# Kernel optimization log

Hardware: AMD Instinct MI355X
Metric: run time of the kernel (lower is better)

The kernel has to match this reference:

```python
import jax, jax.numpy as jnp
import numpy as np

B, S, H, I, E, K = 2, 512, 1024, 4096, 8, 2
LN_EPS = 1e-5


def setup_inputs() -> dict:
    key = jax.random.key(0)
    ks = jax.random.split(key, 5)
    sc = 0.02  # init scale for weights
    return {
        "hidden_states": jax.random.normal(ks[0], (B, S, H), jnp.float32),
        "ln_w": jnp.ones((H,), jnp.float32),
        "ln_b": jnp.zeros((H,), jnp.float32),
        "Wr": jax.random.normal(ks[1], (E, H), jnp.float32) * sc,  # router [out=E, in=H]
        "br": jnp.zeros((E,), jnp.float32),
        "W1": jax.random.normal(ks[2], (E, I, H), jnp.float32) * sc,  # dense1 per expert [out=I, in=H]
        "b1": jnp.zeros((E, I), jnp.float32),
        "W2": jax.random.normal(ks[3], (E, H, I), jnp.float32) * sc,  # dense2 per expert [out=H, in=I]
        "b2": jnp.zeros((E, H), jnp.float32),
    }


def reference(hidden_states, ln_w, ln_b, Wr, br, W1, b1, W2, b2):
    # Eval mode: no jitter noise, no dropout.
    residual = hidden_states
    mu = jnp.mean(hidden_states, axis=-1, keepdims=True)
    var = jnp.mean(jnp.square(hidden_states - mu), axis=-1, keepdims=True)
    x = (hidden_states - mu) * jax.lax.rsqrt(var + LN_EPS) * ln_w + ln_b  # [B,S,H]

    logits = jnp.einsum("bsh,eh->bse", x, Wr) + br  # [B,S,E]
    topw, topi = jax.lax.top_k(logits, K)  # [B,S,K]
    topw = jax.nn.softmax(topw, axis=-1)
    # Combine weights per expert (top-k indices are distinct, so scatter == first-match)
    combine = jnp.sum(jax.nn.one_hot(topi, E, dtype=x.dtype) * topw[..., None], axis=-2)  # [B,S,E]

    # Dense per-expert FFN (reference form of gather-FFN-scatter); combine zeros out unselected experts
    a = jax.nn.gelu(jnp.einsum("bsh,eih->bsei", x, W1) + b1, approximate=False)  # [B,S,E,I]
    y = jnp.einsum("bsei,ehi->bseh", a, W2) + b2  # [B,S,E,H]
    out = residual + jnp.einsum("bse,bseh->bsh", combine, y)

    probs = jax.nn.softmax(logits, axis=-1)
    usage = jnp.mean(probs, axis=(0, 1))  # [E]
    balance_loss = E * jnp.sum(usage * usage) - 1.0
    return out, balance_loss
```

## Files before the change

kernel.cpp:

```cpp
#include <hip/hip_runtime.h>
#include <hip/hip_bf16.h>
#include <math.h>
#include <stdint.h>

#define T_TOK 1024
#define H_DIM 1024
#define I_DIM 4096
#define E_NUM 8
#define NSLOT (2 * T_TOK)
#define WELEM 33554432
#define MAXT 24

typedef __attribute__((ext_vector_type(8))) short bf16x8;
typedef __attribute__((ext_vector_type(4))) float f32x4;

#define MFMA_BF16(a, b, c) __builtin_amdgcn_mfma_f32_16x16x32_bf16(a, b, c, 0, 0, 0)

__device__ __forceinline__ short f2bf(float f) {
  union { float f; unsigned u; } x; x.f = f;
  unsigned r = (x.u + 0x7fffu + ((x.u >> 16) & 1u)) >> 16;
  return (short)r;
}
__device__ __forceinline__ int pack2bf(float a, float b) {
  return ((int)(unsigned short)f2bf(a)) | (((int)f2bf(b)) << 16);
}

typedef __attribute__((address_space(3))) unsigned int as3_u32;
typedef const __attribute__((address_space(1))) unsigned int as1_u32c;
__device__ __forceinline__ void glds16(const void* g, void* l) {
  __builtin_amdgcn_global_load_lds((as1_u32c*)g, (as3_u32*)l, 16, 0, 0);
}

union BBCast { int4 i4; bf16x8 v; };

__device__ __forceinline__ void cvtpack_dev(const float* __restrict__ src,
                                            short* __restrict__ dst,
                                            int bid, int nb, int rsh, int csh) {
  const size_t total8 = ((size_t)E_NUM << (rsh + csh)) >> 3;
  const int kmask = (1 << (csh - 3)) - 1;
  const int nmask = (1 << rsh) - 1;
  for (size_t id = (size_t)bid * 256 + threadIdx.x; id < total8;
       id += (size_t)nb * 256) {
    int k8 = (int)(id & kmask);
    int n = (int)((id >> (csh - 3)) & nmask);
    int e = (int)(id >> (csh - 3 + rsh));
    int k = k8 << 3;
    size_t eoff = (size_t)e << (rsh + csh);
    const float* s = src + eoff + ((size_t)n << csh) + k;
    float4 a = *(const float4*)s;
    float4 b = *(const float4*)(s + 4);
    int4 p;
    p.x = pack2bf(a.x, a.y); p.y = pack2bf(a.z, a.w);
    p.z = pack2bf(b.x, b.y); p.w = pack2bf(b.z, b.w);
    size_t tile = ((size_t)(n >> 7) << (csh - 5)) + (k >> 5);
    *(int4*)(dst + eoff + tile * 4096 + ((n & 127) << 5) + (k & 31)) = p;
  }
}

__global__ __launch_bounds__(256) void k_pre(
    const float* __restrict__ x, const float* __restrict__ ln_w,
    const float* __restrict__ ln_b, const float* __restrict__ Wr,
    const float* __restrict__ br,
    short* __restrict__ xln, int* __restrict__ sel_e, float* __restrict__ sel_w,
    float* __restrict__ probs, float* __restrict__ out,
    const float* __restrict__ W1src, short* __restrict__ w1dst, int ncvt) {
  __shared__ float sx[H_DIM];
  __shared__ float redS[8];
  __shared__ float slog[E_NUM];

  if (blockIdx.x >= T_TOK) {
    cvtpack_dev(W1src, w1dst, blockIdx.x - T_TOK, ncvt, 12, 10);
    return;
  }
  const int t = blockIdx.x;
  const int tid = threadIdx.x;
  const int lane = tid & 63, wid = tid >> 6;

  float4 v = ((const float4*)(x + (size_t)t * H_DIM))[tid];
  ((float4*)(out + (size_t)t * H_DIM))[tid] = v;
  float s = v.x + v.y + v.z + v.w;
  float ss = v.x * v.x + v.y * v.y + v.z * v.z + v.w * v.w;
  for (int o = 32; o > 0; o >>= 1) { s += __shfl_down(s, o); ss += __shfl_down(ss, o); }
  if (lane == 0) { redS[wid] = s; redS[4 + wid] = ss; }
  __syncthreads();
  float st = redS[0] + redS[1] + redS[2] + redS[3];
  float sst = redS[4] + redS[5] + redS[6] + redS[7];
  float mu = st * (1.0f / H_DIM);
  float var = sst * (1.0f / H_DIM) - mu * mu;
  float rs = rsqrtf(var + 1e-5f);

  float4 lw = ((const float4*)ln_w)[tid];
  float4 lb = ((const float4*)ln_b)[tid];
  float4 xn;
  xn.x = (v.x - mu) * rs * lw.x + lb.x;
  xn.y = (v.y - mu) * rs * lw.y + lb.y;
  xn.z = (v.z - mu) * rs * lw.z + lb.z;
  xn.w = (v.w - mu) * rs * lw.w + lb.w;
  sx[4 * tid + 0] = xn.x; sx[4 * tid + 1] = xn.y;
  sx[4 * tid + 2] = xn.z; sx[4 * tid + 3] = xn.w;
  short4 s4;
  s4.x = f2bf(xn.x); s4.y = f2bf(xn.y); s4.z = f2bf(xn.z); s4.w = f2bf(xn.w);
  ((short4*)(xln + (size_t)t * H_DIM))[tid] = s4;
  __syncthreads();

  for (int e = 2 * wid; e < 2 * wid + 2; ++e) {
    float p = 0.f;
    for (int h = lane; h < H_DIM; h += 64) p += sx[h] * Wr[e * H_DIM + h];
    for (int o = 32; o > 0; o >>= 1) p += __shfl_down(p, o);
    if (lane == 0) slog[e] = p + br[e];
  }
  __syncthreads();

  if (tid == 0) {
    float lg[E_NUM];
    for (int e = 0; e < E_NUM; ++e) lg[e] = slog[e];
    int i0 = 0;
    for (int e = 1; e < E_NUM; ++e) if (lg[e] > lg[i0]) i0 = e;
    int i1 = (i0 == 0) ? 1 : 0;
    for (int e = 0; e < E_NUM; ++e) if (e != i0 && lg[e] > lg[i1]) i1 = e;
    float w1e = __expf(lg[i1] - lg[i0]);
    float den = 1.f + w1e;
    sel_e[2 * t] = i0; sel_w[2 * t] = 1.f / den;
    sel_e[2 * t + 1] = i1; sel_w[2 * t + 1] = w1e / den;
    float se = 0.f, pe[E_NUM];
    for (int e = 0; e < E_NUM; ++e) { pe[e] = __expf(lg[e] - lg[i0]); se += pe[e]; }
    float inv = 1.f / se;
    for (int e = 0; e < E_NUM; ++e) probs[t * E_NUM + e] = pe[e] * inv;
  }
}

__global__ __launch_bounds__(512) void k_route(
    const int* __restrict__ sel_e, const float* __restrict__ sel_w,
    const float* __restrict__ probs,
    int* __restrict__ counts, int* __restrict__ basep,
    int* __restrict__ tile_e, int* __restrict__ tile_m0, int* __restrict__ ntiles,
    int* __restrict__ tlist, int* __restrict__ sel_idx,
    float* __restrict__ wslot, float* __restrict__ loss_out) {
  const int wid = threadIdx.x >> 6;
  const int lane = threadIdx.x & 63;
  __shared__ int scnt[E_NUM];
  __shared__ float susage[E_NUM];

  int cnt = 0;
  for (int s0 = 0; s0 < NSLOT; s0 += 64) {
    int s = s0 + lane;
    bool m = (sel_e[s] == wid);
    unsigned long long mk = __ballot(m);
    int pre = __popcll(mk & ((1ULL << lane) - 1ULL));
    if (m) {
      int idx = cnt + pre;
      sel_idx[s] = idx;
      tlist[wid * T_TOK + idx] = s >> 1;
      wslot[wid * T_TOK + idx] = sel_w[s];
    }
    cnt += __popcll(mk);
  }
  if (lane == 0) scnt[wid] = cnt;

  float u = 0.f;
  for (int t = lane; t < T_TOK; t += 64) u += probs[t * E_NUM + wid];
  for (int o = 32; o > 0; o >>= 1) u += __shfl_down(u, o);
  if (lane == 0) susage[wid] = u * (1.0f / T_TOK);
  __syncthreads();

  if (threadIdx.x == 0) {
    int b = 0, nt = 0;
    for (int e = 0; e < E_NUM; ++e) {
      basep[e] = b; counts[e] = scnt[e];
      int te = (scnt[e] + 127) >> 7;
      for (int i = 0; i < te && nt < MAXT; ++i) {
        tile_e[nt] = e; tile_m0[nt] = i * 128; ++nt;
      }
      b += te * 128;
    }
    ntiles[0] = nt;
    float sq = 0.f;
    for (int e = 0; e < E_NUM; ++e) sq += susage[e] * susage[e];
    *loss_out = (float)E_NUM * sq - 1.0f;
  }
}

__global__ __launch_bounds__(256) void k_cvtpack(const float* __restrict__ src,
                                                 short* __restrict__ dst,
                                                 int rsh, int csh) {
  cvtpack_dev(src, dst, blockIdx.x, gridDim.x, rsh, csh);
}

__global__ __launch_bounds__(256) void k_ffn1(
    const short* __restrict__ xln, const short* __restrict__ W1b,
    const float* __restrict__ b1, const int* __restrict__ counts,
    const int* __restrict__ basep,
    const int* __restrict__ tile_e, const int* __restrict__ tile_m0,
    const int* __restrict__ ntiles, const int* __restrict__ tlist,
    short* __restrict__ a_buf,
    const float* __restrict__ W2src, short* __restrict__ w2dst) {
  const int bid = blockIdx.x;
  if (bid >= MAXT * 32) {
    cvtpack_dev(W2src, w2dst, bid - MAXT * 32, gridDim.x - MAXT * 32, 10, 12);
    return;
  }
  const int tileid = bid >> 5;
  if (tileid >= ntiles[0]) return;
  const int e = tile_e[tileid];
  const int m0 = tile_m0[tileid];
  const int cnt = counts[e];
  const int n0 = (bid & 31) * 128;

  __shared__ __align__(16) short As[3][128 * 32];
  __shared__ __align__(16) short Bs[3][128 * 32];

  const int tid = threadIdx.x;
  const int lane = tid & 63, wid = tid >> 6;
  const int wr = wid >> 1, wc = wid & 1;
  const int fr = lane & 15, fq = lane >> 4;

  int r0 = m0 + (tid >> 2); if (r0 >= cnt) r0 = cnt - 1;
  int r1 = m0 + 64 + (tid >> 2); if (r1 >= cnt) r1 = cnt - 1;
  const short* ag0 = xln + (size_t)tlist[e * T_TOK + r0] * H_DIM + (tid & 3) * 8;
  const short* ag1 = xln + (size_t)tlist[e * T_TOK + r1] * H_DIM + (tid & 3) * 8;
  const short* bgp = W1b + ((size_t)e << 22) + ((size_t)(n0 >> 7) * 131072) + tid * 8;

  f32x4 acc[4][4];
#pragma unroll
  for (int i = 0; i < 4; ++i)
#pragma unroll
    for (int j = 0; j < 4; ++j) acc[i][j] = (f32x4)0.f;

#define STAGE(kt, buf)                                          \
  {                                                             \
    glds16(ag0 + (kt) * 32, &As[buf][tid * 8]);                 \
    glds16(ag1 + (kt) * 32, &As[buf][(256 + tid) * 8]);         \
    glds16(bgp + (size_t)(kt) * 4096, &Bs[buf][tid * 8]);       \
    glds16(bgp + (size_t)(kt) * 4096 + 2048,                    \
           &Bs[buf][(256 + tid) * 8]);                          \
  }

  STAGE(0, 0);
  STAGE(1, 1);

  const int KT = H_DIM / 32;
  for (int kt = 0; kt < KT; ++kt) {
    if (kt == KT - 1) {
      asm volatile("s_waitcnt vmcnt(0)" ::: "memory");
    } else {
      asm volatile("s_waitcnt vmcnt(4)" ::: "memory");
    }
    __builtin_amdgcn_s_barrier();
    if (kt + 2 < KT) STAGE(kt + 2, (kt + 2) % 3);
    const int cb = kt % 3;
    bf16x8 af[4], bb[4];
#pragma unroll
    for (int mi = 0; mi < 4; ++mi)
      af[mi] = *(const bf16x8*)&As[cb][(wr * 64 + mi * 16 + fr) * 32 + fq * 8];
#pragma unroll
    for (int ni = 0; ni < 4; ++ni)
      bb[ni] = *(const bf16x8*)&Bs[cb][(wc * 64 + ni * 16 + fr) * 32 + fq * 8];
#pragma unroll
    for (int mi = 0; mi < 4; ++mi)
#pragma unroll
      for (int ni = 0; ni < 4; ++ni)
        acc[mi][ni] = MFMA_BF16(af[mi], bb[ni], acc[mi][ni]);
  }
#undef STAGE

  const size_t T1 = (size_t)(basep[e] + m0) >> 7;
  short* abase = a_buf + T1 * 524288;
  float b1v[4];
#pragma unroll
  for (int ni = 0; ni < 4; ++ni)
    b1v[ni] = b1[e * I_DIM + n0 + wc * 64 + ni * 16 + fr];
#pragma unroll
  for (int mi = 0; mi < 4; ++mi)
#pragma unroll
    for (int j = 0; j < 4; ++j) {
      int r = wr * 64 + mi * 16 + fq * 4 + j;
      if (m0 + r < cnt) {
#pragma unroll
        for (int ni = 0; ni < 4; ++ni) {
          int colg = n0 + wc * 64 + ni * 16 + fr;
          float vv = acc[mi][ni][j] + b1v[ni];
          float g = 0.5f * vv * (1.0f + erff(vv * 0.70710678118654752f));
          abase[(size_t)(colg >> 5) * 4096 + r * 32 + (colg & 31)] = f2bf(g);
        }
      }
    }
}

__global__ __launch_bounds__(256) void k_ffn2(
    const short* __restrict__ a_buf, const short* __restrict__ W2b,
    const float* __restrict__ b2, const int* __restrict__ counts,
    const int* __restrict__ basep,
    const int* __restrict__ tile_e, const int* __restrict__ tile_m0,
    const int* __restrict__ ntiles, const int* __restrict__ tlist,
    const float* __restrict__ wslot, float* __restrict__ out) {
  const int bid = blockIdx.x;
  const int tileid = bid >> 5;
  if (tileid >= ntiles[0]) return;
  const int rem = bid & 31;
  const int kc = rem >> 3;
  const int n0 = (rem & 7) * 128;
  const int e = tile_e[tileid];
  const int m0 = tile_m0[tileid];
  const int cnt = counts[e];

  __shared__ __align__(16) short As[3][128 * 32];
  __shared__ __align__(16) short Bs[3][128 * 32];

  const int tid = threadIdx.x;
  const int lane = tid & 63, wid = tid >> 6;
  const int wr = wid >> 1, wc = wid & 1;
  const int fr = lane & 15, fq = lane >> 4;

  const size_t T1 = (size_t)(basep[e] + m0) >> 7;
  const short* agp = a_buf + T1 * 524288 + (size_t)kc * 131072 + tid * 8;
  const short* bgp = W2b + ((size_t)e << 22) + ((size_t)(n0 >> 7) * 524288) +
                     (size_t)kc * 131072 + tid * 8;

  f32x4 acc[4][4];
#pragma unroll
  for (int i = 0; i < 4; ++i)
#pragma unroll
    for (int j = 0; j < 4; ++j) acc[i][j] = (f32x4)0.f;

#define STAGE(kt, buf)                                          \
  {                                                             \
    glds16(agp + (size_t)(kt) * 4096, &As[buf][tid * 8]);       \
    glds16(agp + (size_t)(kt) * 4096 + 2048,                    \
           &As[buf][(256 + tid) * 8]);                          \
    glds16(bgp + (size_t)(kt) * 4096, &Bs[buf][tid * 8]);       \
    glds16(bgp + (size_t)(kt) * 4096 + 2048,                    \
           &Bs[buf][(256 + tid) * 8]);                          \
  }

  STAGE(0, 0);
  STAGE(1, 1);

  const int KT = 32;
  for (int kt = 0; kt < KT; ++kt) {
    if (kt == KT - 1) {
      asm volatile("s_waitcnt vmcnt(0)" ::: "memory");
    } else {
      asm volatile("s_waitcnt vmcnt(4)" ::: "memory");
    }
    __builtin_amdgcn_s_barrier();
    if (kt + 2 < KT) STAGE(kt + 2, (kt + 2) % 3);
    const int cb = kt % 3;
    bf16x8 af[4], bb[4];
#pragma unroll
    for (int mi = 0; mi < 4; ++mi)
      af[mi] = *(const bf16x8*)&As[cb][(wr * 64 + mi * 16 + fr) * 32 + fq * 8];
#pragma unroll
    for (int ni = 0; ni < 4; ++ni)
      bb[ni] = *(const bf16x8*)&Bs[cb][(wc * 64 + ni * 16 + fr) * 32 + fq * 8];
#pragma unroll
    for (int mi = 0; mi < 4; ++mi)
#pragma unroll
      for (int ni = 0; ni < 4; ++ni)
        acc[mi][ni] = MFMA_BF16(af[mi], bb[ni], acc[mi][ni]);
  }
#undef STAGE

  float b2v[4];
#pragma unroll
  for (int ni = 0; ni < 4; ++ni)
    b2v[ni] = 0.25f * b2[e * H_DIM + n0 + wc * 64 + ni * 16 + fr];
#pragma unroll
  for (int mi = 0; mi < 4; ++mi)
#pragma unroll
    for (int j = 0; j < 4; ++j) {
      int r = wr * 64 + mi * 16 + fq * 4 + j;
      if (m0 + r < cnt) {
        int tok = tlist[e * T_TOK + m0 + r];
        float w = wslot[e * T_TOK + m0 + r];
        float* orow = out + (size_t)tok * H_DIM;
#pragma unroll
        for (int ni = 0; ni < 4; ++ni) {
          int colg = n0 + wc * 64 + ni * 16 + fr;
          atomicAdd(&orow[colg], w * (acc[mi][ni][j] + b2v[ni]));
        }
      }
    }
}

__global__ __launch_bounds__(256) void k_ffn1_f32(
    const short* __restrict__ xln, const float* __restrict__ W1,
    const float* __restrict__ b1, const int* __restrict__ counts,
    const int* __restrict__ basep, const int* __restrict__ tlist,
    short* __restrict__ a_buf) {
  const int e = blockIdx.z;
  const int cnt = counts[e];
  const int m0 = blockIdx.y * 128;
  if (m0 >= cnt) return;
  const int n0 = blockIdx.x * 128;
  __shared__ __align__(16) short As[2][128 * 32];
  __shared__ __align__(16) float Bsf[2][128 * 32];
  const int tid = threadIdx.x;
  const int lane = tid & 63, wid = tid >> 6;
  const int wr = wid >> 1, wc = wid & 1;
  const int fr = lane & 15, fq = lane >> 4;
  int r0 = m0 + (tid >> 2); if (r0 >= cnt) r0 = cnt - 1;
  int r1 = m0 + 64 + (tid >> 2); if (r1 >= cnt) r1 = cnt - 1;
  const short* ag0 = xln + (size_t)tlist[e * T_TOK + r0] * H_DIM + (tid & 3) * 8;
  const short* ag1 = xln + (size_t)tlist[e * T_TOK + r1] * H_DIM + (tid & 3) * 8;
  const int bro = tid >> 3;
  const int bslot = (tid & 7) ^ (bro & 7);
  const float* bg = W1 + ((size_t)e * I_DIM + n0 + bro) * H_DIM + bslot * 4;
  f32x4 acc[4][4];
#pragma unroll
  for (int i = 0; i < 4; ++i)
#pragma unroll
    for (int j = 0; j < 4; ++j) acc[i][j] = (f32x4)0.f;
#define STAGE(kk, buf)                                                      \
  {                                                                         \
    glds16(ag0 + (kk), &As[buf][tid * 8]);                                  \
    glds16(ag1 + (kk), &As[buf][(256 + tid) * 8]);                          \
    _Pragma("unroll") for (int i = 0; i < 4; ++i)                           \
        glds16(bg + (size_t)(i * 32) * H_DIM + (kk),                        \
               &Bsf[buf][(i * 256 + tid) * 4]);                             \
  }
  STAGE(0, 0);
  __syncthreads();
  int cur = 0;
  for (int kt = 0; kt < H_DIM / 32; ++kt) {
    if (kt + 1 < H_DIM / 32) STAGE((kt + 1) * 32, cur ^ 1);
    bf16x8 af[4], bb[4];
#pragma unroll
    for (int mi = 0; mi < 4; ++mi)
      af[mi] = *(const bf16x8*)&As[cur][(wr * 64 + mi * 16 + fr) * 32 + fq * 8];
#pragma unroll
    for (int ni = 0; ni < 4; ++ni) {
      const int row = wc * 64 + ni * 16 + fr;
      const int base = row * 128 + fq * 32;
      const int sw = (row & 7) << 4;
      f32x4 lo = *(const f32x4*)((const char*)&Bsf[cur][0] + (base ^ sw));
      f32x4 hi = *(const f32x4*)((const char*)&Bsf[cur][0] + ((base + 16) ^ sw));
      BBCast c;
      c.i4.x = pack2bf(lo[0], lo[1]); c.i4.y = pack2bf(lo[2], lo[3]);
      c.i4.z = pack2bf(hi[0], hi[1]); c.i4.w = pack2bf(hi[2], hi[3]);
      bb[ni] = c.v;
    }
#pragma unroll
    for (int mi = 0; mi < 4; ++mi)
#pragma unroll
      for (int ni = 0; ni < 4; ++ni)
        acc[mi][ni] = MFMA_BF16(af[mi], bb[ni], acc[mi][ni]);
    __syncthreads();
    cur ^= 1;
  }
#undef STAGE
  const int slot0 = basep[e] + m0;
  float b1v[4];
#pragma unroll
  for (int ni = 0; ni < 4; ++ni)
    b1v[ni] = b1[e * I_DIM + n0 + wc * 64 + ni * 16 + fr];
#pragma unroll
  for (int mi = 0; mi < 4; ++mi)
#pragma unroll
    for (int j = 0; j < 4; ++j) {
      int r = wr * 64 + mi * 16 + fq * 4 + j;
      if (m0 + r < cnt) {
        size_t rowoff = (size_t)(slot0 + r) * I_DIM;
#pragma unroll
        for (int ni = 0; ni < 4; ++ni) {
          int colg = n0 + wc * 64 + ni * 16 + fr;
          float vv = acc[mi][ni][j] + b1v[ni];
          float g = 0.5f * vv * (1.0f + erff(vv * 0.70710678118654752f));
          a_buf[rowoff + colg] = f2bf(g);
        }
      }
    }
}

__global__ __launch_bounds__(256) void k_ffn2_f32(
    const short* __restrict__ a_buf, const float* __restrict__ W2,
    const float* __restrict__ b2, const int* __restrict__ counts,
    const int* __restrict__ basep, const int* __restrict__ tlist,
    const float* __restrict__ wslot, float* __restrict__ out, int lg) {
  const int z = blockIdx.z;
  const int e = z >> lg;
  const int kc = z & ((1 << lg) - 1);
  const int CH = I_DIM >> lg;
  const int cnt = counts[e];
  const int m0 = blockIdx.y * 128;
  if (m0 >= cnt) return;
  const int n0 = blockIdx.x * 128;
  __shared__ __align__(16) short As[2][128 * 32];
  __shared__ __align__(16) float Bsf[2][128 * 32];
  const int tid = threadIdx.x;
  const int lane = tid & 63, wid = tid >> 6;
  const int wr = wid >> 1, wc = wid & 1;
  const int fr = lane & 15, fq = lane >> 4;
  int r0 = m0 + (tid >> 2); if (r0 >= cnt) r0 = cnt - 1;
  int r1 = m0 + 64 + (tid >> 2); if (r1 >= cnt) r1 = cnt - 1;
  const int sb = basep[e];
  const short* ag0 = a_buf + (size_t)(sb + r0) * I_DIM + kc * CH + (tid & 3) * 8;
  const short* ag1 = a_buf + (size_t)(sb + r1) * I_DIM + kc * CH + (tid & 3) * 8;
  const int bro = tid >> 3;
  const int bslot = (tid & 7) ^ (bro & 7);
  const float* bg = W2 + ((size_t)e * H_DIM + n0 + bro) * I_DIM + kc * CH + bslot * 4;
  f32x4 acc[4][4];
#pragma unroll
  for (int i = 0; i < 4; ++i)
#pragma unroll
    for (int j = 0; j < 4; ++j) acc[i][j] = (f32x4)0.f;
#define STAGE(kk, buf)                                                      \
  {                                                                         \
    glds16(ag0 + (kk), &As[buf][tid * 8]);                                  \
    glds16(ag1 + (kk), &As[buf][(256 + tid) * 8]);                          \
    _Pragma("unroll") for (int i = 0; i < 4; ++i)                           \
        glds16(bg + (size_t)(i * 32) * I_DIM + (kk),                        \
               &Bsf[buf][(i * 256 + tid) * 4]);                             \
  }
  STAGE(0, 0);
  __syncthreads();
  const int KT = CH / 32;
  int cur = 0;
  for (int kt = 0; kt < KT; ++kt) {
    if (kt + 1 < KT) STAGE((kt + 1) * 32, cur ^ 1);
    bf16x8 af[4], bb[4];
#pragma unroll
    for (int mi = 0; mi < 4; ++mi)
      af[mi] = *(const bf16x8*)&As[cur][(wr * 64 + mi * 16 + fr) * 32 + fq * 8];
#pragma unroll
    for (int ni = 0; ni < 4; ++ni) {
      const int row = wc * 64 + ni * 16 + fr;
      const int base = row * 128 + fq * 32;
      const int sw = (row & 7) << 4;
      f32x4 lo = *(const f32x4*)((const char*)&Bsf[cur][0] + (base ^ sw));
      f32x4 hi = *(const f32x4*)((const char*)&Bsf[cur][0] + ((base + 16) ^ sw));
      BBCast c;
      c.i4.x = pack2bf(lo[0], lo[1]); c.i4.y = pack2bf(lo[2], lo[3]);
      c.i4.z = pack2bf(hi[0], hi[1]); c.i4.w = pack2bf(hi[2], hi[3]);
      bb[ni] = c.v;
    }
#pragma unroll
    for (int mi = 0; mi < 4; ++mi)
#pragma unroll
      for (int ni = 0; ni < 4; ++ni)
        acc[mi][ni] = MFMA_BF16(af[mi], bb[ni], acc[mi][ni]);
    __syncthreads();
    cur ^= 1;
  }
#undef STAGE
  const float inv = 1.0f / (float)(1 << lg);
  float b2v[4];
#pragma unroll
  for (int ni = 0; ni < 4; ++ni)
    b2v[ni] = inv * b2[e * H_DIM + n0 + wc * 64 + ni * 16 + fr];
#pragma unroll
  for (int mi = 0; mi < 4; ++mi)
#pragma unroll
    for (int j = 0; j < 4; ++j) {
      int r = wr * 64 + mi * 16 + fq * 4 + j;
      if (m0 + r < cnt) {
        int tok = tlist[e * T_TOK + m0 + r];
        float w = wslot[e * T_TOK + m0 + r];
        float* orow = out + (size_t)tok * H_DIM;
#pragma unroll
        for (int ni = 0; ni < 4; ++ni) {
          int colg = n0 + wc * 64 + ni * 16 + fr;
          atomicAdd(&orow[colg], w * (acc[mi][ni][j] + b2v[ni]));
        }
      }
    }
}

extern "C" void kernel_launch(void* const* d_in, const int* in_sizes, int n_in,
                              void* d_out, int out_size, void* d_ws, size_t ws_size,
                              hipStream_t stream) {
  const float* hidden = (const float*)d_in[0];
  const float* ln_w = (const float*)d_in[1];
  const float* ln_b = (const float*)d_in[2];
  const float* Wr = (const float*)d_in[3];
  const float* br = (const float*)d_in[4];
  const float* W1 = (const float*)d_in[5];
  const float* b1 = (const float*)d_in[6];
  const float* W2 = (const float*)d_in[7];
  const float* b2 = (const float*)d_in[8];
  float* out = (float*)d_out;

  char* w = (char*)d_ws;
  int* counts = (int*)(w + 0);
  int* basep = (int*)(w + 64);
  int* ntiles = (int*)(w + 128);
  int* tile_e = (int*)(w + 192);
  int* tile_m0 = (int*)(w + 320);
  float* probs = (float*)(w + 512);
  int* tlist = (int*)(w + 33280);
  int* sel_e = (int*)(w + 66048);
  int* sel_idx = (int*)(w + 74240);
  float* sel_w = (float*)(w + 82432);
  float* wslot = (float*)(w + 90624);
  short* xln = (short*)(w + 131072);
  short* a_buf = (short*)(w + 2228224);
  short* w1_bf = (short*)(w + 27394048);
  short* w2_bf = (short*)(w + 94502912);
  const size_t REQ_SEQ = 94502912;
  const size_t REQ_FUSED = 161611776;

  if (ws_size >= REQ_SEQ) {
    const bool fused = (ws_size >= REQ_FUSED);
    short* w2dst = fused ? w2_bf : w1_bf;
    k_pre<<<T_TOK + 1024, 256, 0, stream>>>(hidden, ln_w, ln_b, Wr, br, xln,
                                            sel_e, sel_w, probs, out, W1, w1_bf, 1024);
    k_route<<<1, 512, 0, stream>>>(sel_e, sel_w, probs, counts, basep,
                                   tile_e, tile_m0, ntiles, tlist, sel_idx,
                                   wslot, out + (size_t)T_TOK * H_DIM);
    if (fused) {
      k_ffn1<<<MAXT * 32 + 256, 256, 0, stream>>>(
          xln, w1_bf, b1, counts, basep, tile_e, tile_m0, ntiles, tlist, a_buf,
          W2, w2_bf);
    } else {
      k_ffn1<<<MAXT * 32, 256, 0, stream>>>(
          xln, w1_bf, b1, counts, basep, tile_e, tile_m0, ntiles, tlist, a_buf,
          nullptr, nullptr);
      k_cvtpack<<<1024, 256, 0, stream>>>(W2, w2dst, 10, 12);
    }
    k_ffn2<<<MAXT * 32, 256, 0, stream>>>(
        a_buf, w2dst, b2, counts, basep, tile_e, tile_m0, ntiles, tlist,
        wslot, out);
  } else {
    k_pre<<<T_TOK, 256, 0, stream>>>(hidden, ln_w, ln_b, Wr, br, xln,
                                     sel_e, sel_w, probs, out, nullptr, nullptr, 0);
    k_route<<<1, 512, 0, stream>>>(sel_e, sel_w, probs, counts, basep,
                                   tile_e, tile_m0, ntiles, tlist, sel_idx,
                                   wslot, out + (size_t)T_TOK * H_DIM);
    const int lg = 2;
    k_ffn1_f32<<<dim3(I_DIM / 128, T_TOK / 128, E_NUM), 256, 0, stream>>>(
        xln, W1, b1, counts, basep, tlist, a_buf);
    k_ffn2_f32<<<dim3(H_DIM / 128, T_TOK / 128, E_NUM << lg), 256, 0, stream>>>(
        a_buf, W2, b2, counts, basep, tlist, wslot, out, lg);
  }
}
```

Before: 217.4 us.

## Replace FFN2 atomic scatter with partial buffers and a token combine kernel

In the fused path, k_ffn2 now writes each K-chunk's partial results to a slot-indexed fp32 buffer (reusing the W1 bf16 area) instead of atomically adding into the output. A new k_combine kernel sums the four partials per selected expert, adds bias and residual, applies the routing weights and writes each output row once. The W2 conversion blocks are also moved to the front of the k_ffn1 grid so they are scheduled first. This removes the float atomics and their contention, at the cost of an extra kernel launch and roughly 50 MB of partial-buffer traffic.

```diff
diff --git a/kernel.cpp b/kernel.cpp
--- a/kernel.cpp
+++ b/kernel.cpp
@@ -8,8 +8,8 @@
 #define I_DIM 4096
 #define E_NUM 8
 #define NSLOT (2 * T_TOK)
-#define WELEM 33554432
 #define MAXT 24
+#define SLOTP 3072
 
 typedef __attribute__((ext_vector_type(8))) short bf16x8;
 typedef __attribute__((ext_vector_type(4))) float f32x4;
@@ -193,18 +193,19 @@
     const int* __restrict__ tile_e, const int* __restrict__ tile_m0,
     const int* __restrict__ ntiles, const int* __restrict__ tlist,
     short* __restrict__ a_buf,
-    const float* __restrict__ W2src, short* __restrict__ w2dst) {
+    const float* __restrict__ W2src, short* __restrict__ w2dst, int nc2) {
   const int bid = blockIdx.x;
-  if (bid >= MAXT * 32) {
-    cvtpack_dev(W2src, w2dst, bid - MAXT * 32, gridDim.x - MAXT * 32, 10, 12);
+  if (bid < nc2) {
+    cvtpack_dev(W2src, w2dst, bid, nc2, 10, 12);
     return;
   }
-  const int tileid = bid >> 5;
+  const int gbid = bid - nc2;
+  const int tileid = gbid >> 5;
   if (tileid >= ntiles[0]) return;
   const int e = tile_e[tileid];
   const int m0 = tile_m0[tileid];
   const int cnt = counts[e];
-  const int n0 = (bid & 31) * 128;
+  const int n0 = (gbid & 31) * 128;
 
   __shared__ __align__(16) short As[3][128 * 32];
   __shared__ __align__(16) short Bs[3][128 * 32];
@@ -292,7 +293,8 @@
     const int* __restrict__ basep,
     const int* __restrict__ tile_e, const int* __restrict__ tile_m0,
     const int* __restrict__ ntiles, const int* __restrict__ tlist,
-    const float* __restrict__ wslot, float* __restrict__ out) {
+    const float* __restrict__ wslot, float* __restrict__ y_part,
+    float* __restrict__ out) {
   const int bid = blockIdx.x;
   const int tileid = bid >> 5;
   if (tileid >= ntiles[0]) return;
@@ -360,26 +362,76 @@
   }
 #undef STAGE
 
-  float b2v[4];
-#pragma unroll
-  for (int ni = 0; ni < 4; ++ni)
-    b2v[ni] = 0.25f * b2[e * H_DIM + n0 + wc * 64 + ni * 16 + fr];
-#pragma unroll
-  for (int mi = 0; mi < 4; ++mi)
-#pragma unroll
-    for (int j = 0; j < 4; ++j) {
-      int r = wr * 64 + mi * 16 + fq * 4 + j;
-      if (m0 + r < cnt) {
-        int tok = tlist[e * T_TOK + m0 + r];
-        float w = wslot[e * T_TOK + m0 + r];
-        float* orow = out + (size_t)tok * H_DIM;
-#pragma unroll
-        for (int ni = 0; ni < 4; ++ni) {
-          int colg = n0 + wc * 64 + ni * 16 + fr;
-          atomicAdd(&orow[colg], w * (acc[mi][ni][j] + b2v[ni]));
+  const int slot0 = basep[e] + m0;
+  if (y_part) {
+    float* yp = y_part + (size_t)kc * ((size_t)SLOTP * H_DIM);
+#pragma unroll
+    for (int mi = 0; mi < 4; ++mi)
+#pragma unroll
+      for (int j = 0; j < 4; ++j) {
+        int r = wr * 64 + mi * 16 + fq * 4 + j;
+        if (m0 + r < cnt) {
+          size_t rowoff = (size_t)(slot0 + r) * H_DIM;
+#pragma unroll
+          for (int ni = 0; ni < 4; ++ni) {
+            int colg = n0 + wc * 64 + ni * 16 + fr;
+            yp[rowoff + colg] = acc[mi][ni][j];
+          }
         }
       }
-    }
+  } else {
+    float b2v[4];
+#pragma unroll
+    for (int ni = 0; ni < 4; ++ni)
+      b2v[ni] = 0.25f * b2[e * H_DIM + n0 + wc * 64 + ni * 16 + fr];
+#pragma unroll
+    for (int mi = 0; mi < 4; ++mi)
+#pragma unroll
+      for (int j = 0; j < 4; ++j) {
+        int r = wr * 64 + mi * 16 + fq * 4 + j;
+        if (m0 + r < cnt) {
+          int tok = tlist[e * T_TOK + m0 + r];
+          float w = wslot[e * T_TOK + m0 + r];
+          float* orow = out + (size_t)tok * H_DIM;
+#pragma unroll
+          for (int ni = 0; ni < 4; ++ni) {
+            int colg = n0 + wc * 64 + ni * 16 + fr;
+            atomicAdd(&orow[colg], w * (acc[mi][ni][j] + b2v[ni]));
+          }
+        }
+      }
+  }
+}
+
+__global__ __launch_bounds__(256) void k_combine(
+    const float* __restrict__ hidden, const float* __restrict__ y_part,
+    const float* __restrict__ b2, const int* __restrict__ basep,
+    const int* __restrict__ sel_e, const int* __restrict__ sel_idx,
+    const float* __restrict__ sel_w, float* __restrict__ out) {
+  const int t = blockIdx.x;
+  const int tid = threadIdx.x;
+  int e0 = sel_e[2 * t], e1 = sel_e[2 * t + 1];
+  size_t s0 = (size_t)basep[e0] + sel_idx[2 * t];
+  size_t s1 = (size_t)basep[e1] + sel_idx[2 * t + 1];
+  float w0 = sel_w[2 * t], w1 = sel_w[2 * t + 1];
+  const size_t TY = (size_t)SLOTP * H_DIM;
+  float4 y0 = make_float4(0.f, 0.f, 0.f, 0.f);
+  float4 y1 = make_float4(0.f, 0.f, 0.f, 0.f);
+  for (int kc = 0; kc < 4; ++kc) {
+    float4 p0 = ((const float4*)(y_part + kc * TY + s0 * H_DIM))[tid];
+    float4 p1 = ((const float4*)(y_part + kc * TY + s1 * H_DIM))[tid];
+    y0.x += p0.x; y0.y += p0.y; y0.z += p0.z; y0.w += p0.w;
+    y1.x += p1.x; y1.y += p1.y; y1.z += p1.z; y1.w += p1.w;
+  }
+  float4 be0 = ((const float4*)(b2 + (size_t)e0 * H_DIM))[tid];
+  float4 be1 = ((const float4*)(b2 + (size_t)e1 * H_DIM))[tid];
+  float4 r = ((const float4*)(hidden + (size_t)t * H_DIM))[tid];
+  float4 o;
+  o.x = r.x + w0 * (y0.x + be0.x) + w1 * (y1.x + be1.x);
+  o.y = r.y + w0 * (y0.y + be0.y) + w1 * (y1.y + be1.y);
+  o.z = r.z + w0 * (y0.z + be0.z) + w1 * (y1.z + be1.z);
+  o.w = r.w + w0 * (y0.w + be0.w) + w1 * (y1.w + be1.w);
+  ((float4*)(out + (size_t)t * H_DIM))[tid] = o;
 }
 
 __global__ __launch_bounds__(256) void k_ffn1_f32(
@@ -595,30 +647,35 @@
   short* a_buf = (short*)(w + 2228224);
   short* w1_bf = (short*)(w + 27394048);
   short* w2_bf = (short*)(w + 94502912);
+  float* y_part = (float*)w1_bf;
   const size_t REQ_SEQ = 94502912;
   const size_t REQ_FUSED = 161611776;
 
   if (ws_size >= REQ_SEQ) {
     const bool fused = (ws_size >= REQ_FUSED);
-    short* w2dst = fused ? w2_bf : w1_bf;
     k_pre<<<T_TOK + 1024, 256, 0, stream>>>(hidden, ln_w, ln_b, Wr, br, xln,
                                             sel_e, sel_w, probs, out, W1, w1_bf, 1024);
     k_route<<<1, 512, 0, stream>>>(sel_e, sel_w, probs, counts, basep,
                                    tile_e, tile_m0, ntiles, tlist, sel_idx,
                                    wslot, out + (size_t)T_TOK * H_DIM);
     if (fused) {
-      k_ffn1<<<MAXT * 32 + 256, 256, 0, stream>>>(
+      k_ffn1<<<256 + MAXT * 32, 256, 0, stream>>>(
           xln, w1_bf, b1, counts, basep, tile_e, tile_m0, ntiles, tlist, a_buf,
-          W2, w2_bf);
+          W2, w2_bf, 256);
+      k_ffn2<<<MAXT * 32, 256, 0, stream>>>(
+          a_buf, w2_bf, b2, counts, basep, tile_e, tile_m0, ntiles, tlist,
+          wslot, y_part, out);
+      k_combine<<<T_TOK, 256, 0, stream>>>(hidden, y_part, b2, basep,
+                                           sel_e, sel_idx, sel_w, out);
     } else {
       k_ffn1<<<MAXT * 32, 256, 0, stream>>>(
           xln, w1_bf, b1, counts, basep, tile_e, tile_m0, ntiles, tlist, a_buf,
-          nullptr, nullptr);
-      k_cvtpack<<<1024, 256, 0, stream>>>(W2, w2dst, 10, 12);
-    }
-    k_ffn2<<<MAXT * 32, 256, 0, stream>>>(
-        a_buf, w2dst, b2, counts, basep, tile_e, tile_m0, ntiles, tlist,
-        wslot, out);
+          nullptr, nullptr, 0);
+      k_cvtpack<<<1024, 256, 0, stream>>>(W2, w1_bf, 10, 12);
+      k_ffn2<<<MAXT * 32, 256, 0, stream>>>(
+          a_buf, w1_bf, b2, counts, basep, tile_e, tile_m0, ntiles, tlist,
+          wslot, nullptr, out);
+    }
   } else {
     k_pre<<<T_TOK, 256, 0, stream>>>(hidden, ln_w, ln_b, Wr, br, xln,
                                      sel_e, sel_w, probs, out, nullptr, nullptr, 0);
```

Result: faster. 207.9 us (-4.4%).
